# Optimization experiments

Measured on AMD Instinct MI355X. Metric: run time of the kernel, lower is better.

The kernel has to match this reference:

```python
import jax, jax.numpy as jnp
import numpy as np

B, HG, WG, D, NH, K = 4, 32, 32, 768, 12, 7
HD = D // NH  # 64


def _neigh_idx(H, W, k):
    # NATTEN semantics: 7x7 window centered at the query, shifted (clamped)
    # at borders so every query has exactly k*k neighbors.
    si = np.clip(np.arange(H) - k // 2, 0, H - k)  # [H] window row starts
    sj = np.clip(np.arange(W) - k // 2, 0, W - k)  # [W] window col starts
    ri = si[:, None] + np.arange(k)[None, :]       # [H, k]
    cj = sj[:, None] + np.arange(k)[None, :]       # [W, k]
    idx = ri[:, None, :, None] * W + cj[None, :, None, :]  # [H, W, k, k]
    return jnp.asarray(idx.reshape(H * W, k * k), dtype=jnp.int32)


def setup_inputs() -> dict:
    key = jax.random.key(0)
    ks = jax.random.split(key, 3)
    s = D ** -0.5
    return {
        "x": jax.random.normal(ks[0], (B, HG * WG, D), dtype=jnp.float32),
        "qkv_w": jax.random.normal(ks[1], (3 * D, D), dtype=jnp.float32) * s,
        "qkv_b": jnp.zeros((3 * D,), dtype=jnp.float32),
        "proj_w": jax.random.normal(ks[2], (D, D), dtype=jnp.float32) * s,
        "proj_b": jnp.zeros((D,), dtype=jnp.float32),
    }


def reference(x, qkv_w, qkv_b, proj_w, proj_b):
    b, n, d = x.shape  # n == HG*WG
    idx = _neigh_idx(HG, WG, K)  # [n, K*K] flat neighbor token indices

    qkv = x @ qkv_w.T + qkv_b                      # [b, n, 3d]
    q, k, v = jnp.split(qkv, 3, axis=-1)
    q = q.reshape(b, n, NH, HD) * (HD ** -0.5)     # [b, n, h, hd]
    k = k.reshape(b, n, NH, HD)
    v = v.reshape(b, n, NH, HD)

    kn = jnp.take(k, idx, axis=1)                  # [b, n, 49, h, hd]
    vn = jnp.take(v, idx, axis=1)                  # [b, n, 49, h, hd]

    scores = jnp.einsum('bnhd,bnkhd->bnhk', q, kn)  # [b, n, h, 49]
    attn = jax.nn.softmax(scores, axis=-1)
    out = jnp.einsum('bnhk,bnkhd->bnhd', attn, vn).reshape(b, n, d)
    return out @ proj_w.T + proj_b
```

## Files before the change

### kernel.cpp

```cpp
#include <hip/hip_runtime.h>


typedef __bf16 bf16x8 __attribute__((ext_vector_type(8)));
typedef short s16x4 __attribute__((ext_vector_type(4)));
typedef float f32x4 __attribute__((ext_vector_type(4)));

__device__ __forceinline__ unsigned short f2bf(float f) {
  unsigned u = __float_as_uint(f);
  u += 0x7fffu + ((u >> 16) & 1u);
  return (unsigned short)(u >> 16);
}

template <typename T>
__device__ __forceinline__ void gld_lds16(const T* g, T* l) {
  __builtin_amdgcn_global_load_lds((const __attribute__((address_space(1))) void*)g,
                                   (__attribute__((address_space(3))) void*)l, 16, 0, 0);
}

__global__ void cvt_kernel(const float* __restrict__ x, const float* __restrict__ w1,
                           const float* __restrict__ w2, unsigned short* __restrict__ xo,
                           unsigned short* __restrict__ w1o, unsigned short* __restrict__ w2o) {
  const int n1 = 4096 * 768 / 4;
  const int n2 = 2304 * 768 / 4;
  const int n3 = 768 * 768 / 4;
  int i = blockIdx.x * 256 + threadIdx.x;
  float4 v;
  unsigned short* dst;
  int o;
  if (i < n1) {
    o = i; v = ((const float4*)x)[o]; dst = xo;
  } else if (i < n1 + n2) {
    o = i - n1; v = ((const float4*)w1)[o]; dst = w1o;
  } else if (i < n1 + n2 + n3) {
    o = i - n1 - n2; v = ((const float4*)w2)[o]; dst = w2o;
  } else {
    return;
  }
  ushort4 r;
  r.x = f2bf(v.x); r.y = f2bf(v.y); r.z = f2bf(v.z); r.w = f2bf(v.w);
  ((ushort4*)dst)[o] = r;
}

template <int MODE, int BM, int BN>
__global__ __launch_bounds__(256) void gemm_bt(const unsigned short* __restrict__ A,
                                               const unsigned short* __restrict__ Bm,
                                               const float* __restrict__ bias,
                                               unsigned short* __restrict__ obf,
                                               unsigned short* __restrict__ vtout,
                                               float* __restrict__ of32,
                                               int M, int N, int Kd) {
  constexpr int RA = BM / 64, RB = BN / 64;
  constexpr int MI = BM / 32, NI = BN / 32;
  constexpr int NB = (MODE == 0) ? 4 : 5;
  constexpr int DEPTH = NB - 1;
  __shared__ __align__(16) unsigned short sA[NB][BM * 32];
  __shared__ __align__(16) unsigned short sB[NB][BN * 32];
  const int tid = threadIdx.x;
  const int lane = tid & 63;
  const int wv = tid >> 6;

  constexpr int HX = (MODE == 0) ? 9 : 6;
  constexpr int HY = (MODE == 0) ? 8 : 16;
  const int lin = blockIdx.y * gridDim.x + blockIdx.x;
  const int xcd = lin & 7, rrr = lin >> 3;
  const int bx = (xcd & 1) * HX + rrr % HX;
  const int by = (xcd >> 1) * HY + rrr / HX;
  const int m0 = by * BM, n0 = bx * BN;

  const int wrow = (wv >> 1) * (BM / 2), wcol = (wv & 1) * (BN / 2);
  const int lr = lane & 15, lq = lane >> 4;
  const int rchunk = (lq ^ ((lr >> 1) & 3)) * 8;

  f32x4 acc[MI][NI] = {};

  const int schunk = ((tid & 3) ^ ((tid >> 3) & 3)) * 8;
  const unsigned short* gA = A + (size_t)(m0 + (tid >> 2)) * Kd + schunk;
  const unsigned short* gB = Bm + (size_t)(n0 + (tid >> 2)) * Kd + schunk;

  const int NS = Kd >> 5;

#define STAGE_TILE(tile, bufidx)                                                          \
  do {                                                                                    \
    const int _off = (tile) * 32;                                                         \
    unsigned short* _dA = sA[(bufidx)];                                                   \
    unsigned short* _dB = sB[(bufidx)];                                                   \
    _Pragma("unroll")                                                                     \
    for (int _r = 0; _r < RA; ++_r)                                                       \
      gld_lds16(gA + (size_t)(_r * 64) * Kd + _off, _dA + _r * 2048 + tid * 8);           \
    _Pragma("unroll")                                                                     \
    for (int _r = 0; _r < RB; ++_r)                                                       \
      gld_lds16(gB + (size_t)(_r * 64) * Kd + _off, _dB + _r * 2048 + tid * 8);           \
  } while (0)

#pragma unroll
  for (int t = 0; t < DEPTH; ++t) STAGE_TILE(t, t);
  __builtin_amdgcn_sched_barrier(0);
  if constexpr (MODE == 0) asm volatile("s_waitcnt vmcnt(8) lgkmcnt(0)" ::: "memory");
  else                     asm volatile("s_waitcnt vmcnt(6) lgkmcnt(0)" ::: "memory");
  __builtin_amdgcn_s_barrier();

  int rb = 0, sb = DEPTH;
  for (int step = 0; step < NS; ++step) {
    const unsigned short* cA = sA[rb];
    const unsigned short* cB = sB[rb];
    bf16x8 af[MI], bfr[NI];
#pragma unroll
    for (int t = 0; t < MI; ++t) af[t] = *(const bf16x8*)(cA + (wrow + t * 16 + lr) * 32 + rchunk);
#pragma unroll
    for (int t = 0; t < NI; ++t) bfr[t] = *(const bf16x8*)(cB + (wcol + t * 16 + lr) * 32 + rchunk);

    if (step + DEPTH < NS) STAGE_TILE(step + DEPTH, sb);

#pragma unroll
    for (int im = 0; im < MI; ++im)
#pragma unroll
      for (int in = 0; in < NI; ++in)
        acc[im][in] = __builtin_amdgcn_mfma_f32_16x16x32_bf16(af[im], bfr[in], acc[im][in], 0, 0, 0);

    __builtin_amdgcn_sched_barrier(0);
    if constexpr (MODE == 0) {
      if (step + 3 < NS)      asm volatile("s_waitcnt vmcnt(8) lgkmcnt(0)" ::: "memory");
      else if (step + 2 < NS) asm volatile("s_waitcnt vmcnt(4) lgkmcnt(0)" ::: "memory");
      else                    asm volatile("s_waitcnt vmcnt(0) lgkmcnt(0)" ::: "memory");
    } else {
      if (step + 4 < NS)      asm volatile("s_waitcnt vmcnt(6) lgkmcnt(0)" ::: "memory");
      else if (step + 3 < NS) asm volatile("s_waitcnt vmcnt(4) lgkmcnt(0)" ::: "memory");
      else if (step + 2 < NS) asm volatile("s_waitcnt vmcnt(2) lgkmcnt(0)" ::: "memory");
      else                    asm volatile("s_waitcnt vmcnt(0) lgkmcnt(0)" ::: "memory");
    }
    __builtin_amdgcn_s_barrier();
    rb = (rb + 1 == NB) ? 0 : rb + 1;
    sb = (sb + 1 == NB) ? 0 : sb + 1;
  }
#undef STAGE_TILE

  if (MODE == 0) {
    const int sidx = n0 / 768;
    if (sidx == 2) {
#pragma unroll
      for (int im = 0; im < MI; ++im) {
#pragma unroll
        for (int in = 0; in < NI; ++in) {
          int gn = n0 + wcol + in * 16 + lr;
          int rem = gn - 1536;
          int hh = rem >> 6, dd = gn & 63;
          float bsv = bias[gn];
          int gm0 = m0 + wrow + im * 16 + lq * 4;
          ushort4 pk;
          pk.x = f2bf(acc[im][in][0] + bsv);
          pk.y = f2bf(acc[im][in][1] + bsv);
          pk.z = f2bf(acc[im][in][2] + bsv);
          pk.w = f2bf(acc[im][in][3] + bsv);
          *(ushort4*)(vtout + (size_t)(hh * 64 + dd) * 4096 + gm0) = pk;
        }
      }
    } else {
      const float scale = (sidx == 0) ? 0.18033688f : 1.0f;
#pragma unroll
      for (int im = 0; im < MI; ++im) {
#pragma unroll
        for (int in = 0; in < NI; ++in) {
          int gn = n0 + wcol + in * 16 + lr;
          int rem = gn - sidx * 768;
          int hh = rem >> 6, dd = gn & 63;
          float bsv = bias[gn];
#pragma unroll
          for (int r = 0; r < 4; ++r) {
            int gm = m0 + wrow + im * 16 + lq * 4 + r;
            float val = (acc[im][in][r] + bsv) * scale;
            obf[((size_t)(sidx * 12 + hh) * 4096 + gm) * 64 + dd] = f2bf(val);
          }
        }
      }
    }
  } else {
#pragma unroll
    for (int im = 0; im < MI; ++im) {
#pragma unroll
      for (int in = 0; in < NI; ++in) {
        int gn = n0 + wcol + in * 16 + lr;
        float bsv = bias[gn];
#pragma unroll
        for (int r = 0; r < 4; ++r) {
          int gm = m0 + wrow + im * 16 + lq * 4 + r;
          of32[(size_t)gm * N + gn] = acc[im][in][r] + bsv;
        }
      }
    }
  }
}

__global__ __launch_bounds__(256, 2) void natten_kernel(const unsigned short* __restrict__ qkvt,
                                                        unsigned short* __restrict__ aout) {
  __shared__ __align__(16) unsigned short sQ[64 * 64];
  __shared__ __align__(16) unsigned short sK[256 * 64];
  __shared__ __align__(16) unsigned short sVt[64 * 256];
  const int h = blockIdx.x, ip = blockIdx.y, b = blockIdx.z;
  const int i0 = ip * 2;
  const int tid = threadIdx.x, lane = tid & 63, wv = tid >> 6;
  const int lg = lane >> 4, lm = lane & 15;
  int si0 = i0 - 3; si0 = si0 < 0 ? 0 : si0; if (si0 > 25) si0 = 25;
  const int gb = b * 1024;
  const unsigned short* Qg = qkvt + ((size_t)h * 4096 + gb + i0 * 32) * 64;
  const unsigned short* Kg = qkvt + ((size_t)(12 + h) * 4096 + gb) * 64;
  const unsigned short* Vg = qkvt + (size_t)24 * 4096 * 64 + (size_t)h * 64 * 4096 + gb;

#pragma unroll
  for (int it = 0; it < 2; ++it) {
    int f = it * 256 + tid;
    int q = f >> 3, c16 = f & 7;
    uint4 v = *(const uint4*)(Qg + q * 64 + c16 * 8);
    int s = q & 15;
    *(uint2*)(sQ + q * 64 + ((((c16 << 1)) ^ s) << 2)) = make_uint2(v.x, v.y);
    *(uint2*)(sQ + q * 64 + ((((c16 << 1) | 1) ^ s) << 2)) = make_uint2(v.z, v.w);
  }
#pragma unroll
  for (int it = 0; it < 8; ++it) {
    int f = it * 256 + tid;
    int t = f >> 3, c16 = f & 7;
    int wr = t >> 5, c = t & 31;
    int row = si0 + wr; if (row > 31) row = 31;
    uint4 v = *(const uint4*)(Kg + (row * 32 + c) * 64 + c16 * 8);
    int s = t & 15;
    *(uint2*)(sK + t * 64 + ((((c16 << 1)) ^ s) << 2)) = make_uint2(v.x, v.y);
    *(uint2*)(sK + t * 64 + ((((c16 << 1) | 1) ^ s) << 2)) = make_uint2(v.z, v.w);
  }
#pragma unroll
  for (int it = 0; it < 8; ++it) {
    int f = it * 256 + tid;
    int d = f >> 5, tc16 = f & 31;
    int wr = tc16 >> 2;
    int row = si0 + wr; if (row > 31) row = 31;
    uint4 v = *(const uint4*)(Vg + (size_t)d * 4096 + row * 32 + (tc16 & 3) * 8);
    int s = d & 15;
    *(uint2*)(sVt + d * 256 + ((((tc16 << 1)) ^ s) << 2)) = make_uint2(v.x, v.y);
    *(uint2*)(sVt + d * 256 + ((((tc16 << 1) | 1) ^ s) << 2)) = make_uint2(v.z, v.w);
  }
  __syncthreads();

  const int row_sel = wv >> 1;
  const int jhalf = wv & 1;
  const int i = i0 + row_sel;
  int si_w = i - 3; si_w = si_w < 0 ? 0 : si_w; if (si_w > 25) si_w = 25;
  const int toff = (si_w - si0) * 32;
  const int j = jhalf * 16 + lm;
  int sj = j - 3; sj = sj < 0 ? 0 : sj; if (sj > 25) sj = 25;

  float madd[2][4];
#pragma unroll
  for (int p = 0; p < 2; ++p)
#pragma unroll
    for (int r = 0; r < 4; ++r) {
      int c = p * 16 + lg * 4 + r;
      madd[p][r] = (c >= sj && c <= sj + 6) ? 0.f : -1e30f;
    }

  s16x4 qf[4];
  const int qrow = row_sel * 32 + j;
#pragma unroll
  for (int ks = 0; ks < 4; ++ks)
    qf[ks] = *(const s16x4*)(sQ + qrow * 64 + ((((ks << 2) + lg) ^ (qrow & 15)) << 2));

  f32x4 accS[14];
#pragma unroll
  for (int tt = 0; tt < 14; ++tt) {
    f32x4 a = {0.f, 0.f, 0.f, 0.f};
    const int trow = toff + tt * 16 + lm;
    const unsigned short* kr = sK + trow * 64;
    const int sw = trow & 15;
#pragma unroll
    for (int ks = 0; ks < 4; ++ks) {
      s16x4 kf = *(const s16x4*)(kr + ((((ks << 2) + lg) ^ sw) << 2));
      a = __builtin_amdgcn_mfma_f32_16x16x16bf16_1k(kf, qf[ks], a, 0, 0, 0);
    }
    accS[tt] = a;
  }

  float mx = -3e38f;
#pragma unroll
  for (int tt = 0; tt < 14; ++tt)
#pragma unroll
    for (int r = 0; r < 4; ++r) {
      float v = accS[tt][r] + madd[tt & 1][r];
      accS[tt][r] = v;
      mx = fmaxf(mx, v);
    }
  mx = fmaxf(mx, __shfl_xor(mx, 16, 64));
  mx = fmaxf(mx, __shfl_xor(mx, 32, 64));
  float sum = 0.f;
#pragma unroll
  for (int tt = 0; tt < 14; ++tt)
#pragma unroll
    for (int r = 0; r < 4; ++r) {
      float p = exp2f(accS[tt][r] - mx);
      accS[tt][r] = p;
      sum += p;
    }
  sum += __shfl_xor(sum, 16, 64);
  sum += __shfl_xor(sum, 32, 64);
  const float inv = 1.f / sum;

  s16x4 pf[14];
#pragma unroll
  for (int tt = 0; tt < 14; ++tt) {
    union { unsigned u[2]; s16x4 v; } pk;
    pk.u[0] = ((unsigned)f2bf(accS[tt][1]) << 16) | f2bf(accS[tt][0]);
    pk.u[1] = ((unsigned)f2bf(accS[tt][3]) << 16) | f2bf(accS[tt][2]);
    pf[tt] = pk.v;
  }

  f32x4 accO[4] = {};
  const int choff = toff >> 2;
#pragma unroll
  for (int tt = 0; tt < 14; ++tt) {
    const int c8 = choff + tt * 4 + lg;
#pragma unroll
    for (int nt = 0; nt < 4; ++nt) {
      const int d = nt * 16 + lm;
      s16x4 vf = *(const s16x4*)(sVt + d * 256 + ((c8 ^ (d & 15)) << 2));
      accO[nt] = __builtin_amdgcn_mfma_f32_16x16x16bf16_1k(pf[tt], vf, accO[nt], 0, 0, 0);
    }
  }

  float invr[4];
#pragma unroll
  for (int r = 0; r < 4; ++r) invr[r] = __shfl(inv, lg * 4 + r, 64);

  const int tokbase = gb + i * 32 + jhalf * 16;
#pragma unroll
  for (int nt = 0; nt < 4; ++nt)
#pragma unroll
    for (int r = 0; r < 4; ++r) {
      int tok = tokbase + lg * 4 + r;
      aout[(size_t)tok * 768 + h * 64 + nt * 16 + lm] = f2bf(accO[nt][r] * invr[r]);
    }
}

extern "C" void kernel_launch(void* const* d_in, const int* in_sizes, int n_in,
                              void* d_out, int out_size, void* d_ws, size_t ws_size,
                              hipStream_t stream) {
  const float* x      = (const float*)d_in[0];
  const float* qkv_w  = (const float*)d_in[1];
  const float* qkv_b  = (const float*)d_in[2];
  const float* proj_w = (const float*)d_in[3];
  const float* proj_b = (const float*)d_in[4];
  char* ws = (char*)d_ws;

  unsigned short* xb    = (unsigned short*)(ws);
  unsigned short* wqkv  = (unsigned short*)(ws + 6291456);
  unsigned short* wproj = (unsigned short*)(ws + 9830400);
  unsigned short* qkvt  = (unsigned short*)(ws + 11010048);
  unsigned short* attnb = (unsigned short*)(ws + 29884416);
  unsigned short* vt    = qkvt + (size_t)24 * 4096 * 64;
  float* out = (float*)d_out;

  cvt_kernel<<<5376, 256, 0, stream>>>(x, qkv_w, proj_w, xb, wqkv, wproj);
  gemm_bt<0, 128, 128><<<dim3(18, 32), 256, 0, stream>>>(xb, wqkv, qkv_b, qkvt, vt, nullptr, 4096, 2304, 768);
  natten_kernel<<<dim3(12, 16, 4), 256, 0, stream>>>(qkvt, attnb);
  gemm_bt<1, 64, 64><<<dim3(12, 64), 256, 0, stream>>>(attnb, wproj, proj_b, nullptr, nullptr, out, 4096, 768, 768);
}
```

Measured before the change: 136.6 us.

## Replace QKV GEMM with 256x256-tile 8-wave kernel using swizzled LDS

Adds a dedicated QKV projection kernel that uses 256x256 output tiles, 512 threads (8 waves), a BK=64 double-buffered LDS pipeline with XOR-swizzled layout, interleaved prefetch across MFMA phases, setprio around MFMAs, and an XCD-aware block remap. The 144 blocks cover 2304x4096 in one wave on the device, replacing the 576-block 128x128 generic gemm. The goal is more operand reuse per LDS load and fewer bank conflicts, at the cost of fewer blocks than CUs and high register pressure from 32 accumulators per lane. The old MODE 0 epilogue in the generic GEMM is removed.

Result: no change. 136.5 us (-0.1%).

```diff
diff --git a/kernel.cpp b/kernel.cpp
--- a/kernel.cpp
+++ b/kernel.cpp
@@ -41,6 +41,128 @@
   ((ushort4*)dst)[o] = r;
 }
 
+__global__ __launch_bounds__(512, 2) void gemm_qkv8(const unsigned short* __restrict__ A,
+                                                    const unsigned short* __restrict__ Bm,
+                                                    const float* __restrict__ bias,
+                                                    unsigned short* __restrict__ obf,
+                                                    unsigned short* __restrict__ vtout) {
+  __shared__ __align__(16) unsigned short sA[2][256 * 64];
+  __shared__ __align__(16) unsigned short sB[2][256 * 64];
+  const int tid = threadIdx.x, lane = tid & 63, wv = tid >> 6;
+  const int wr = wv >> 2, wc = wv & 3;
+  const int lr = lane & 15, lq = lane >> 4;
+
+  const int lin = blockIdx.x;
+  const int wgid = (lin & 7) * 18 + (lin >> 3);
+  const int bx = wgid % 9, by = wgid / 9;
+  const int m0 = by * 256, n0 = bx * 256;
+
+  const int srow = tid >> 3;
+  const int sc8 = (tid & 7) * 8;
+  const int scl8 = (((tid & 7) ^ ((tid >> 3) & 7))) * 8;
+  const unsigned short* gA = A + (size_t)(m0 + srow) * 768 + scl8;
+  const unsigned short* gB = Bm + (size_t)(n0 + srow) * 768 + scl8;
+  const int ldst = srow * 64 + sc8;
+
+  f32x4 acc[8][4] = {};
+
+#define STG(t, p)                                                                     \
+  do {                                                                                \
+    unsigned short* dA = sA[(t) & 1];                                                 \
+    unsigned short* dB = sB[(t) & 1];                                                 \
+    const int ko = (t) * 64;                                                          \
+    gld_lds16(gA + (size_t)((p) * 128) * 768 + ko, dA + ((p) * 128) * 64 + ldst);     \
+    gld_lds16(gA + (size_t)((p) * 128 + 64) * 768 + ko, dA + ((p) * 128 + 64) * 64 + ldst); \
+    gld_lds16(gB + (size_t)((p) * 128) * 768 + ko, dB + ((p) * 128) * 64 + ldst);     \
+    gld_lds16(gB + (size_t)((p) * 128 + 64) * 768 + ko, dB + ((p) * 128 + 64) * 64 + ldst); \
+  } while (0)
+
+  STG(0, 0);
+  STG(0, 1);
+  __builtin_amdgcn_sched_barrier(0);
+  asm volatile("s_waitcnt vmcnt(0) lgkmcnt(0)" ::: "memory");
+  __builtin_amdgcn_s_barrier();
+
+  for (int t = 0; t < 12; ++t) {
+    const unsigned short* cA = sA[t & 1];
+    const unsigned short* cB = sB[t & 1];
+    bf16x8 bfr[4][2];
+#pragma unroll
+    for (int nf = 0; nf < 4; ++nf)
+#pragma unroll
+      for (int ks = 0; ks < 2; ++ks)
+        bfr[nf][ks] = *(const bf16x8*)(cB + (wc * 64 + nf * 16 + lr) * 64 +
+                                       (((ks * 4 + lq) ^ (lr & 7)) << 3));
+#pragma unroll
+    for (int ph = 0; ph < 4; ++ph) {
+      bf16x8 af[2][2];
+#pragma unroll
+      for (int i = 0; i < 2; ++i)
+#pragma unroll
+        for (int ks = 0; ks < 2; ++ks)
+          af[i][ks] = *(const bf16x8*)(cA + (wr * 128 + (ph * 2 + i) * 16 + lr) * 64 +
+                                       (((ks * 4 + lq) ^ (lr & 7)) << 3));
+      if (ph < 2 && t + 1 < 12) STG(t + 1, ph);
+      __builtin_amdgcn_s_barrier();
+      __builtin_amdgcn_s_setprio(1);
+#pragma unroll
+      for (int i = 0; i < 2; ++i)
+#pragma unroll
+        for (int nf = 0; nf < 4; ++nf)
+#pragma unroll
+          for (int ks = 0; ks < 2; ++ks)
+            acc[ph * 2 + i][nf] = __builtin_amdgcn_mfma_f32_16x16x32_bf16(
+                af[i][ks], bfr[nf][ks], acc[ph * 2 + i][nf], 0, 0, 0);
+      __builtin_amdgcn_s_setprio(0);
+      if (ph == 3) {
+        __builtin_amdgcn_sched_barrier(0);
+        if (t + 1 < 12) asm volatile("s_waitcnt vmcnt(0)" ::: "memory");
+      }
+      __builtin_amdgcn_s_barrier();
+    }
+  }
+#undef STG
+
+  const int sidx = n0 / 768;
+  if (sidx == 2) {
+#pragma unroll
+    for (int mf = 0; mf < 8; ++mf) {
+#pragma unroll
+      for (int nf = 0; nf < 4; ++nf) {
+        int gn = n0 + wc * 64 + nf * 16 + lr;
+        int rem = gn - 1536;
+        int hh = rem >> 6, dd = gn & 63;
+        float bsv = bias[gn];
+        int gm0 = m0 + wr * 128 + mf * 16 + lq * 4;
+        ushort4 pk;
+        pk.x = f2bf(acc[mf][nf][0] + bsv);
+        pk.y = f2bf(acc[mf][nf][1] + bsv);
+        pk.z = f2bf(acc[mf][nf][2] + bsv);
+        pk.w = f2bf(acc[mf][nf][3] + bsv);
+        *(ushort4*)(vtout + (size_t)(hh * 64 + dd) * 4096 + gm0) = pk;
+      }
+    }
+  } else {
+    const float scale = (sidx == 0) ? 0.18033688f : 1.0f;
+#pragma unroll
+    for (int mf = 0; mf < 8; ++mf) {
+#pragma unroll
+      for (int nf = 0; nf < 4; ++nf) {
+        int gn = n0 + wc * 64 + nf * 16 + lr;
+        int rem = gn - sidx * 768;
+        int hh = rem >> 6, dd = gn & 63;
+        float bsv = bias[gn];
+#pragma unroll
+        for (int r = 0; r < 4; ++r) {
+          int gm = m0 + wr * 128 + mf * 16 + lq * 4 + r;
+          float val = (acc[mf][nf][r] + bsv) * scale;
+          obf[((size_t)(sidx * 12 + hh) * 4096 + gm) * 64 + dd] = f2bf(val);
+        }
+      }
+    }
+  }
+}
+
 template <int MODE, int BM, int BN>
 __global__ __launch_bounds__(256) void gemm_bt(const unsigned short* __restrict__ A,
                                                const unsigned short* __restrict__ Bm,
@@ -135,44 +257,6 @@
 #undef STAGE_TILE
 
   if (MODE == 0) {
-    const int sidx = n0 / 768;
-    if (sidx == 2) {
-#pragma unroll
-      for (int im = 0; im < MI; ++im) {
-#pragma unroll
-        for (int in = 0; in < NI; ++in) {
-          int gn = n0 + wcol + in * 16 + lr;
-          int rem = gn - 1536;
-          int hh = rem >> 6, dd = gn & 63;
-          float bsv = bias[gn];
-          int gm0 = m0 + wrow + im * 16 + lq * 4;
-          ushort4 pk;
-          pk.x = f2bf(acc[im][in][0] + bsv);
-          pk.y = f2bf(acc[im][in][1] + bsv);
-          pk.z = f2bf(acc[im][in][2] + bsv);
-          pk.w = f2bf(acc[im][in][3] + bsv);
-          *(ushort4*)(vtout + (size_t)(hh * 64 + dd) * 4096 + gm0) = pk;
-        }
-      }
-    } else {
-      const float scale = (sidx == 0) ? 0.18033688f : 1.0f;
-#pragma unroll
-      for (int im = 0; im < MI; ++im) {
-#pragma unroll
-        for (int in = 0; in < NI; ++in) {
-          int gn = n0 + wcol + in * 16 + lr;
-          int rem = gn - sidx * 768;
-          int hh = rem >> 6, dd = gn & 63;
-          float bsv = bias[gn];
-#pragma unroll
-          for (int r = 0; r < 4; ++r) {
-            int gm = m0 + wrow + im * 16 + lq * 4 + r;
-            float val = (acc[im][in][r] + bsv) * scale;
-            obf[((size_t)(sidx * 12 + hh) * 4096 + gm) * 64 + dd] = f2bf(val);
-          }
-        }
-      }
-    }
   } else {
 #pragma unroll
     for (int im = 0; im < MI; ++im) {
@@ -355,7 +439,7 @@
   float* out = (float*)d_out;
 
   cvt_kernel<<<5376, 256, 0, stream>>>(x, qkv_w, proj_w, xb, wqkv, wproj);
-  gemm_bt<0, 128, 128><<<dim3(18, 32), 256, 0, stream>>>(xb, wqkv, qkv_b, qkvt, vt, nullptr, 4096, 2304, 768);
+  gemm_qkv8<<<144, 512, 0, stream>>>(xb, wqkv, qkv_b, qkvt, vt);
   natten_kernel<<<dim3(12, 16, 4), 256, 0, stream>>>(qkvt, attnb);
   gemm_bt<1, 64, 64><<<dim3(12, 64), 256, 0, stream>>>(attnb, wproj, proj_b, nullptr, nullptr, out, 4096, 768, 768);
 }
```
